# Performance work log

Measured on AMD Instinct MI355X. Metric: run time of the kernel, lower is better.

## Reference

```python
import jax, jax.numpy as jnp
import numpy as np

TOPK = 2
EPS = 1e-6  # RMSNorm epsilon


def setup_inputs() -> dict:
    key = jax.random.key(0)
    ks = jax.random.split(key, 8)
    b, t, d, h, n = 2, 1024, 1024, 2048, 16
    x = jax.random.normal(ks[0], (b, t, d), dtype=jnp.float32)
    router_w = jax.random.normal(ks[1], (n, d), dtype=jnp.float32) * (1.0 / np.sqrt(d))
    router_bias = jnp.zeros((n,), dtype=jnp.float32)
    bank_mag = jax.random.normal(ks[2], (n, d, h), dtype=jnp.float32) * (1.0 / np.sqrt(d))
    bank_freq = jax.random.uniform(ks[3], (n, d, h), dtype=jnp.float32, minval=0.5, maxval=2.0) * (1.0 / np.sqrt(d))
    bank_phase = jax.random.uniform(ks[4], (n, h), dtype=jnp.float32, minval=-0.3, maxval=0.3)
    bank_down = jax.random.normal(ks[5], (n, h, d), dtype=jnp.float32) * (1.0 / np.sqrt(h))
    norm_w = jnp.ones((d,), dtype=jnp.float32)
    return {
        'x': x, 'router_w': router_w, 'router_bias': router_bias,
        'bank_mag': bank_mag, 'bank_freq': bank_freq, 'bank_phase': bank_phase,
        'bank_down': bank_down, 'norm_w': norm_w,
    }


def reference(x, router_w, router_bias, bank_mag, bank_freq, bank_phase, bank_down, norm_w):
    b, t, d = x.shape
    # Router: scores [b,t,n], top-k selection, softmax over selected logits
    scores = jnp.einsum('btd,nd->btn', x, router_w) + router_bias
    topv, topi = jax.lax.top_k(scores, TOPK)            # [b,t,k]
    weights = jax.nn.softmax(topv, axis=-1)             # [b,t,k]

    fx = x.reshape(b * t, d)                            # [T,d]
    # Dense per-expert compute (mathematically identical to per-token gather+bmm):
    mag = jnp.einsum('td,ndh->tnh', fx, bank_mag)       # [T,n,h]
    freq = jnp.einsum('td,ndh->tnh', fx, bank_freq)     # [T,n,h]
    hidden = jnp.tanh(mag) * jnp.cos(jax.nn.softplus(freq) + 0.1 + bank_phase[None, :, :])
    out_all = jnp.einsum('tnh,nhd->tnd', hidden, bank_down)  # [T,n,d]

    # Gather the top-k expert outputs per token and combine with routing weights
    ti = topi.reshape(b * t, TOPK)                      # [T,k]
    sel = jnp.take_along_axis(out_all, ti[:, :, None], axis=1)  # [T,k,d]
    out = jnp.einsum('tkd,tk->td', sel, weights.reshape(b * t, TOPK)).reshape(b, t, d)

    # RMSNorm
    out = out * jax.lax.rsqrt(jnp.mean(out * out, axis=-1, keepdims=True) + EPS) * norm_w
    return out
```

## Files before the change

kernel.cpp:

```cpp
#include <hip/hip_runtime.h>
#include <hip/hip_bf16.h>
#include <cstdint>
#include <cstddef>

#define TT 2048
#define DD 1024
#define HH 2048
#define NE 16
#define WM128 48
#define BW35 35

typedef __bf16 bf16x8 __attribute__((ext_vector_type(8)));
typedef float f32x4 __attribute__((ext_vector_type(4)));

__device__ __forceinline__ unsigned short f2bf(float f) {
  union { float f; unsigned u; } v; v.f = f;
  unsigned r = (v.u + 0x7FFFu + ((v.u >> 16) & 1u)) >> 16;
  return (unsigned short)r;
}
__device__ __forceinline__ float bf2f(unsigned short s) {
  union { unsigned u; float f; } v; v.u = ((unsigned)s) << 16;
  return v.f;
}
__device__ __forceinline__ unsigned packbf(float lo, float hi) {
  return (unsigned)f2bf(lo) | ((unsigned)f2bf(hi) << 16);
}

__device__ __forceinline__ void gl_lds16(const void* g, void* l) {
  __builtin_amdgcn_global_load_lds(
      (const __attribute__((address_space(1))) unsigned int*)g,
      (__attribute__((address_space(3))) unsigned int*)l, 16, 0, 0);
}

union U4 { unsigned int u[4]; bf16x8 v; };

__global__ __launch_bounds__(256) void k_router(
    const float* __restrict__ x, const float* __restrict__ rw,
    const float* __restrict__ rb, int* __restrict__ cnt,
    int* __restrict__ list_tok, int* __restrict__ rec,
    float* __restrict__ wrec, unsigned short* __restrict__ xbf) {
  const int t = blockIdx.x;
  __shared__ float xs[DD];
  __shared__ float part[256];
  __shared__ float sc[NE];
  const float* xr = x + (size_t)t * DD;
  for (int i = threadIdx.x; i < DD; i += 256) xs[i] = xr[i];
  __syncthreads();
  {
    int i = threadIdx.x * 4;
    ushort4 o = { f2bf(xs[i]), f2bf(xs[i + 1]), f2bf(xs[i + 2]), f2bf(xs[i + 3]) };
    *reinterpret_cast<ushort4*>(xbf + (size_t)t * DD + i) = o;
  }
  const int e = threadIdx.x >> 4, j = threadIdx.x & 15;
  const float* w = rw + (size_t)e * DD;
  float s = 0.f;
  for (int i = j; i < DD; i += 16) s += xs[i] * w[i];
  part[threadIdx.x] = s;
  __syncthreads();
  if (threadIdx.x < NE) {
    float v = rb[threadIdx.x];
    #pragma unroll
    for (int q = 0; q < 16; ++q) v += part[threadIdx.x * 16 + q];
    sc[threadIdx.x] = v;
  }
  __syncthreads();
  if (threadIdx.x == 0) {
    int e1 = 0; float v1 = sc[0];
    #pragma unroll
    for (int q = 1; q < NE; ++q) { if (sc[q] > v1) { v1 = sc[q]; e1 = q; } }
    int e2 = -1; float v2 = -3.4e38f;
    #pragma unroll
    for (int q = 0; q < NE; ++q) {
      if (q != e1 && sc[q] > v2) { v2 = sc[q]; e2 = q; }
    }
    float ex = expf(v2 - v1);
    float w1 = 1.f / (1.f + ex);
    float w2 = ex / (1.f + ex);
    int p1 = atomicAdd(&cnt[e1], 1);
    int p2 = atomicAdd(&cnt[e2], 1);
    list_tok[e1 * TT + p1] = t;
    list_tok[e2 * TT + p2] = t;
    rec[t * 4 + 0] = e1; rec[t * 4 + 1] = p1;
    rec[t * 4 + 2] = e2; rec[t * 4 + 3] = p2;
    wrec[t * 2 + 0] = w1; wrec[t * 2 + 1] = w2;
  }
}

__global__ void k_sched(const int* __restrict__ cnt, int* __restrict__ work128,
                        int* __restrict__ woff) {
  if (threadIdx.x == 0) {
    int o = 0, n1 = 0;
    for (int e = 0; e < NE; ++e) {
      int ce = cnt[e];
      int a = (ce + 127) >> 7;
      for (int mb = 0; mb < a; ++mb) { work128[n1 * 2] = e; work128[n1 * 2 + 1] = mb; ++n1; }
      woff[e] = o; o += ce;
    }
    for (int q = n1; q < WM128; ++q) { work128[q * 2] = -1; work128[q * 2 + 1] = 0; }
  }
}

__global__ __launch_bounds__(256, 2) void k_up(
    const unsigned short* __restrict__ xbf,
    const float* __restrict__ bmag,
    const float* __restrict__ bfreq,
    const float* __restrict__ bphase,
    const int* __restrict__ cnt, const int* __restrict__ list_tok,
    const int* __restrict__ work, const int* __restrict__ woff,
    unsigned short* __restrict__ hid) {
  const int e = work[blockIdx.x * 2 + 0];
  if (e < 0) return;
  const int mt = work[blockIdx.x * 2 + 1];
  const int nt = blockIdx.y;
  const int ce = cnt[e];
  const int off = woff[e];
  __shared__ unsigned short As[2][128][64];
  __shared__ unsigned int BuM[2][64 * BW35];
  __shared__ unsigned int BuF[2][64 * BW35];
  __shared__ int toks[128];
  const int tid = threadIdx.x;
  if (tid < 128) {
    int r = mt * 128 + tid;
    toks[tid] = list_tok[e * TT + (r < ce ? r : ce - 1)];
  }
  __syncthreads();
  const int w = tid >> 6, l = tid & 63;
  const int lhi = l >> 3, llo = l & 7;
  size_t abase[4]; int aoff[4];
  #pragma unroll
  for (int j = 0; j < 4; ++j) {
    int seg = w * 4 + j;
    int r = seg * 8 + lhi;
    abase[j] = (size_t)toks[r] * DD + (size_t)((llo ^ (r & 7)) * 8);
    aoff[j] = seg * 512 + l * 8;
  }
  const int n0 = nt * 64;
  const float* srcM = bmag  + (size_t)e * DD * HH + n0 + 4 * (tid & 15);
  const float* srcF = bfreq + (size_t)e * DD * HH + n0 + 4 * (tid & 15);
  int q2s[2], bw[2][4];
  #pragma unroll
  for (int s = 0; s < 2; ++s) {
    int idx = s * 256 + tid;
    int q2 = idx >> 4;
    q2s[s] = q2;
    #pragma unroll
    for (int i = 0; i < 4; ++i) bw[s][i] = (4 * (tid & 15) + i) * BW35 + q2;
  }
  const int wm = (w >> 1) * 64, wn = (w & 1) * 32;
  const int lr = l & 15, kg = l >> 4;
  const f32x4 zero = {0.f, 0.f, 0.f, 0.f};
  f32x4 accM[4][2], accF[4][2];
  #pragma unroll
  for (int a = 0; a < 4; ++a)
    #pragma unroll
    for (int b = 0; b < 2; ++b) { accM[a][b] = zero; accF[a][b] = zero; }

  float4 rm0[2], rm1[2], rf0[2], rf1[2];
  auto loadB = [&](int kt) {
    #pragma unroll
    for (int s = 0; s < 2; ++s) {
      const float* pM = srcM + (size_t)(kt * 64 + 2 * q2s[s]) * HH;
      const float* pF = srcF + (size_t)(kt * 64 + 2 * q2s[s]) * HH;
      rm0[s] = *reinterpret_cast<const float4*>(pM);
      rm1[s] = *reinterpret_cast<const float4*>(pM + HH);
      rf0[s] = *reinterpret_cast<const float4*>(pF);
      rf1[s] = *reinterpret_cast<const float4*>(pF + HH);
    }
  };
  auto writeB = [&](int buf) {
    #pragma unroll
    for (int s = 0; s < 2; ++s) {
      const float* m0 = reinterpret_cast<const float*>(&rm0[s]);
      const float* m1 = reinterpret_cast<const float*>(&rm1[s]);
      const float* f0 = reinterpret_cast<const float*>(&rf0[s]);
      const float* f1 = reinterpret_cast<const float*>(&rf1[s]);
      #pragma unroll
      for (int i = 0; i < 4; ++i) {
        BuM[buf][bw[s][i]] = packbf(m0[i], m1[i]);
        BuF[buf][bw[s][i]] = packbf(f0[i], f1[i]);
      }
    }
  };

  loadB(0);
  #pragma unroll
  for (int j = 0; j < 4; ++j) gl_lds16(xbf + abase[j], &As[0][0][0] + aoff[j]);
  writeB(0);
  __syncthreads();
  int buf = 0;
  for (int kt = 0; kt < DD / 64; ++kt) {
    const bool more = (kt + 1) < DD / 64;
    if (more) {
      #pragma unroll
      for (int j = 0; j < 4; ++j)
        gl_lds16(xbf + abase[j] + (kt + 1) * 64, &As[buf ^ 1][0][0] + aoff[j]);
      loadB(kt + 1);
    }
    #pragma unroll
    for (int ks = 0; ks < 2; ++ks) {
      bf16x8 av[4];
      #pragma unroll
      for (int fm = 0; fm < 4; ++fm) {
        int row = wm + fm * 16 + lr;
        int c = (ks * 4 + kg) ^ (row & 7);
        av[fm] = *reinterpret_cast<const bf16x8*>(&As[buf][row][c * 8]);
      }
      U4 tm[2], tf[2];
      #pragma unroll
      for (int fn = 0; fn < 2; ++fn) {
        const int nb = (wn + fn * 16 + lr) * BW35 + ks * 16 + kg * 4;
        #pragma unroll
        for (int j2 = 0; j2 < 4; ++j2) {
          tm[fn].u[j2] = BuM[buf][nb + j2];
          tf[fn].u[j2] = BuF[buf][nb + j2];
        }
      }
      #pragma unroll
      for (int fm = 0; fm < 4; ++fm)
        #pragma unroll
        for (int fn = 0; fn < 2; ++fn) {
          accM[fm][fn] = __builtin_amdgcn_mfma_f32_16x16x32_bf16(av[fm], tm[fn].v, accM[fm][fn], 0, 0, 0);
          accF[fm][fn] = __builtin_amdgcn_mfma_f32_16x16x32_bf16(av[fm], tf[fn].v, accF[fm][fn], 0, 0, 0);
        }
    }
    if (more) writeB(buf ^ 1);
    __syncthreads();
    buf ^= 1;
  }
  #pragma unroll
  for (int fn = 0; fn < 2; ++fn) {
    const int ng = n0 + wn + fn * 16 + lr;
    const float ph = bphase[e * HH + ng] + 0.1f;
    #pragma unroll
    for (int fm = 0; fm < 4; ++fm) {
      #pragma unroll
      for (int jj = 0; jj < 4; ++jj) {
        int m = mt * 128 + wm + fm * 16 + kg * 4 + jj;
        if (m < ce) {
          float mv = accM[fm][fn][jj];
          float fv = accF[fm][fn][jj];
          float exn = __expf(-fabsf(fv));
          float sp = fmaxf(fv, 0.f) + __logf(1.f + exn);
          float t2 = __expf(2.f * mv);
          float th = 1.f - 2.f / (t2 + 1.f);
          float hv = th * __cosf(sp + ph);
          hid[(size_t)(off + m) * HH + ng] = f2bf(hv);
        }
      }
    }
  }
}

__global__ __launch_bounds__(256, 3) void k_down(
    const unsigned short* __restrict__ hid,
    const float* __restrict__ bdown,
    const int* __restrict__ cnt,
    const int* __restrict__ work, const int* __restrict__ woff,
    unsigned short* __restrict__ op) {
  const int e = work[blockIdx.x * 2 + 0];
  if (e < 0) return;
  const int mt = work[blockIdx.x * 2 + 1];
  const int nt = blockIdx.y;
  const int ce = cnt[e];
  const int off = woff[e];
  __shared__ unsigned short As[2][128][64];
  __shared__ unsigned int Bu[2][64 * BW35];
  const int tid = threadIdx.x;
  const int w = tid >> 6, l = tid & 63;
  const int lhi = l >> 3, llo = l & 7;
  size_t abase[4]; int aoff[4];
  #pragma unroll
  for (int j = 0; j < 4; ++j) {
    int seg = w * 4 + j;
    int r = seg * 8 + lhi;
    int gr = mt * 128 + r; if (gr >= ce) gr = ce - 1;
    abase[j] = (size_t)(off + gr) * HH + (size_t)((llo ^ (r & 7)) * 8);
    aoff[j] = seg * 512 + l * 8;
  }
  const int n0 = nt * 64;
  const float* srcD = bdown + (size_t)e * HH * DD + n0 + 4 * (tid & 15);
  int q2s[2], bw[2][4];
  #pragma unroll
  for (int s = 0; s < 2; ++s) {
    int idx = s * 256 + tid;
    int q2 = idx >> 4;
    q2s[s] = q2;
    #pragma unroll
    for (int i = 0; i < 4; ++i) bw[s][i] = (4 * (tid & 15) + i) * BW35 + q2;
  }
  const int wm = (w >> 1) * 64, wn = (w & 1) * 32;
  const int lr = l & 15, kg = l >> 4;
  const f32x4 zero = {0.f, 0.f, 0.f, 0.f};
  f32x4 acc[4][2];
  #pragma unroll
  for (int a = 0; a < 4; ++a)
    #pragma unroll
    for (int b = 0; b < 2; ++b) acc[a][b] = zero;

  float4 rd0[2], rd1[2];
  auto loadB = [&](int kt) {
    #pragma unroll
    for (int s = 0; s < 2; ++s) {
      const float* pD = srcD + (size_t)(kt * 64 + 2 * q2s[s]) * DD;
      rd0[s] = *reinterpret_cast<const float4*>(pD);
      rd1[s] = *reinterpret_cast<const float4*>(pD + DD);
    }
  };
  auto writeB = [&](int buf) {
    #pragma unroll
    for (int s = 0; s < 2; ++s) {
      const float* d0 = reinterpret_cast<const float*>(&rd0[s]);
      const float* d1 = reinterpret_cast<const float*>(&rd1[s]);
      #pragma unroll
      for (int i = 0; i < 4; ++i) Bu[buf][bw[s][i]] = packbf(d0[i], d1[i]);
    }
  };

  loadB(0);
  #pragma unroll
  for (int j = 0; j < 4; ++j) gl_lds16(hid + abase[j], &As[0][0][0] + aoff[j]);
  writeB(0);
  __syncthreads();
  int buf = 0;
  for (int kt = 0; kt < HH / 64; ++kt) {
    const bool more = (kt + 1) < HH / 64;
    if (more) {
      #pragma unroll
      for (int j = 0; j < 4; ++j)
        gl_lds16(hid + abase[j] + (kt + 1) * 64, &As[buf ^ 1][0][0] + aoff[j]);
      loadB(kt + 1);
    }
    #pragma unroll
    for (int ks = 0; ks < 2; ++ks) {
      bf16x8 av[4];
      #pragma unroll
      for (int fm = 0; fm < 4; ++fm) {
        int row = wm + fm * 16 + lr;
        int c = (ks * 4 + kg) ^ (row & 7);
        av[fm] = *reinterpret_cast<const bf16x8*>(&As[buf][row][c * 8]);
      }
      U4 t[2];
      #pragma unroll
      for (int fn = 0; fn < 2; ++fn) {
        const int nb = (wn + fn * 16 + lr) * BW35 + ks * 16 + kg * 4;
        #pragma unroll
        for (int j2 = 0; j2 < 4; ++j2) t[fn].u[j2] = Bu[buf][nb + j2];
      }
      #pragma unroll
      for (int fm = 0; fm < 4; ++fm)
        #pragma unroll
        for (int fn = 0; fn < 2; ++fn)
          acc[fm][fn] = __builtin_amdgcn_mfma_f32_16x16x32_bf16(av[fm], t[fn].v, acc[fm][fn], 0, 0, 0);
    }
    if (more) writeB(buf ^ 1);
    __syncthreads();
    buf ^= 1;
  }
  #pragma unroll
  for (int fn = 0; fn < 2; ++fn) {
    const int ng = n0 + wn + fn * 16 + lr;
    #pragma unroll
    for (int fm = 0; fm < 4; ++fm) {
      #pragma unroll
      for (int jj = 0; jj < 4; ++jj) {
        int m = mt * 128 + wm + fm * 16 + kg * 4 + jj;
        if (m < ce)
          op[(size_t)(off + m) * DD + ng] = f2bf(acc[fm][fn][jj]);
      }
    }
  }
}

__global__ __launch_bounds__(256) void k_norm(
    const unsigned short* __restrict__ op, const int* __restrict__ woff,
    const int* __restrict__ rec, const float* __restrict__ wrec,
    const float* __restrict__ nw, float* __restrict__ out) {
  const int t = blockIdx.x;
  const int tid = threadIdx.x;
  __shared__ float red[4];
  const int e1 = rec[t * 4 + 0], p1 = rec[t * 4 + 1];
  const int e2 = rec[t * 4 + 2], p2 = rec[t * 4 + 3];
  const float w1 = wrec[t * 2 + 0], w2 = wrec[t * 2 + 1];
  const unsigned short* pa = op + (size_t)(woff[e1] + p1) * DD;
  const unsigned short* pb = op + (size_t)(woff[e2] + p2) * DD;
  float v[4]; float ss = 0.f;
  #pragma unroll
  for (int q = 0; q < 4; ++q) {
    int i = q * 256 + tid;
    v[q] = w1 * bf2f(pa[i]) + w2 * bf2f(pb[i]);
    ss += v[q] * v[q];
  }
  #pragma unroll
  for (int o = 32; o > 0; o >>= 1) ss += __shfl_xor(ss, o);
  if ((tid & 63) == 0) red[tid >> 6] = ss;
  __syncthreads();
  const float tot = red[0] + red[1] + red[2] + red[3];
  const float scl = rsqrtf(tot * (1.f / DD) + 1e-6f);
  #pragma unroll
  for (int q = 0; q < 4; ++q) {
    int i = q * 256 + tid;
    out[(size_t)t * DD + i] = v[q] * scl * nw[i];
  }
}

extern "C" void kernel_launch(void* const* d_in, const int* in_sizes, int n_in,
                              void* d_out, int out_size, void* d_ws, size_t ws_size,
                              hipStream_t stream) {
  const float* x      = (const float*)d_in[0];
  const float* rw     = (const float*)d_in[1];
  const float* rb     = (const float*)d_in[2];
  const float* bmag   = (const float*)d_in[3];
  const float* bfreq  = (const float*)d_in[4];
  const float* bphase = (const float*)d_in[5];
  const float* bdown  = (const float*)d_in[6];
  const float* nw     = (const float*)d_in[7];
  float* out = (float*)d_out;
  char* ws = (char*)d_ws;
  const size_t MB = 1024 * 1024;
  int*   cnt    = (int*)(ws + 0);
  int*   work1  = (int*)(ws + 128);
  int*   woff   = (int*)(ws + 2048);
  int*   list   = (int*)(ws + 4096);
  int*   rec    = (int*)(ws + 139264);
  float* wrec   = (float*)(ws + 172032);
  unsigned short* xbf = (unsigned short*)(ws + 1 * MB);
  unsigned short* hid = (unsigned short*)(ws + 5 * MB);
  unsigned short* op  = (unsigned short*)(ws + 21 * MB);

  hipMemsetAsync(cnt, 0, 64, stream);
  k_router<<<TT, 256, 0, stream>>>(x, rw, rb, cnt, list, rec, wrec, xbf);
  k_sched<<<1, 64, 0, stream>>>(cnt, work1, woff);
  k_up<<<dim3(WM128, HH / 64), 256, 0, stream>>>(xbf, bmag, bfreq, bphase,
                                                 cnt, list, work1, woff, hid);
  k_down<<<dim3(WM128, DD / 64), 256, 0, stream>>>(hid, bdown, cnt, work1, woff, op);
  k_norm<<<TT, 256, 0, stream>>>(op, woff, rec, wrec, nw, out);
}
```

Baseline: 294.7 us.

## Prefetch weight tiles two stages ahead with ping-pong registers and vmcnt barriers

Both expert GEMM kernels (up-projection mag/freq and down-projection) now keep two register sets of fp32 weight tiles, so global loads run two k-steps ahead instead of one. The loop is unrolled by two, alternating LDS buffers. A custom barrier waits only until the oldest loads complete (partial vmcnt) instead of draining all outstanding memory operations, so later prefetches stay in flight across the barrier. This costs more VGPRs for the extra staging registers and relies on hand-counted vmcnt values that must match the issue order.

```diff
diff --git a/kernel.cpp b/kernel.cpp
--- a/kernel.cpp
+++ b/kernel.cpp
@@ -33,6 +33,15 @@
 }
 
 union U4 { unsigned int u[4]; bf16x8 v; };
+
+#define BARRIER_N(N)                                            \
+  do {                                                          \
+    asm volatile("s_waitcnt vmcnt(" #N ")" ::: "memory");       \
+    asm volatile("s_waitcnt lgkmcnt(0)" ::: "memory");          \
+    __builtin_amdgcn_sched_barrier(0);                          \
+    __builtin_amdgcn_s_barrier();                               \
+    __builtin_amdgcn_sched_barrier(0);                          \
+  } while (0)
 
 __global__ __launch_bounds__(256) void k_router(
     const float* __restrict__ x, const float* __restrict__ rw,
@@ -137,14 +146,14 @@
   const int n0 = nt * 64;
   const float* srcM = bmag  + (size_t)e * DD * HH + n0 + 4 * (tid & 15);
   const float* srcF = bfreq + (size_t)e * DD * HH + n0 + 4 * (tid & 15);
-  int q2s[2], bw[2][4];
+  int q2s[2], bwv[2][4];
   #pragma unroll
   for (int s = 0; s < 2; ++s) {
     int idx = s * 256 + tid;
     int q2 = idx >> 4;
     q2s[s] = q2;
     #pragma unroll
-    for (int i = 0; i < 4; ++i) bw[s][i] = (4 * (tid & 15) + i) * BW35 + q2;
+    for (int i = 0; i < 4; ++i) bwv[s][i] = (4 * (tid & 15) + i) * BW35 + q2;
   }
   const int wm = (w >> 1) * 64, wn = (w & 1) * 32;
   const int lr = l & 15, kg = l >> 4;
@@ -155,47 +164,65 @@
     #pragma unroll
     for (int b = 0; b < 2; ++b) { accM[a][b] = zero; accF[a][b] = zero; }
 
-  float4 rm0[2], rm1[2], rf0[2], rf1[2];
-  auto loadB = [&](int kt) {
+  float4 Am0[2], Am1[2], Af0[2], Af1[2];
+  float4 Bm0[2], Bm1[2], Bf0[2], Bf1[2];
+
+  auto glA = [&](int kt, int buf) {
+    #pragma unroll
+    for (int j = 0; j < 4; ++j)
+      gl_lds16(xbf + abase[j] + kt * 64, &As[buf][0][0] + aoff[j]);
+  };
+  auto loadBA = [&](int kt) {
     #pragma unroll
     for (int s = 0; s < 2; ++s) {
       const float* pM = srcM + (size_t)(kt * 64 + 2 * q2s[s]) * HH;
       const float* pF = srcF + (size_t)(kt * 64 + 2 * q2s[s]) * HH;
-      rm0[s] = *reinterpret_cast<const float4*>(pM);
-      rm1[s] = *reinterpret_cast<const float4*>(pM + HH);
-      rf0[s] = *reinterpret_cast<const float4*>(pF);
-      rf1[s] = *reinterpret_cast<const float4*>(pF + HH);
-    }
-  };
-  auto writeB = [&](int buf) {
-    #pragma unroll
-    for (int s = 0; s < 2; ++s) {
-      const float* m0 = reinterpret_cast<const float*>(&rm0[s]);
-      const float* m1 = reinterpret_cast<const float*>(&rm1[s]);
-      const float* f0 = reinterpret_cast<const float*>(&rf0[s]);
-      const float* f1 = reinterpret_cast<const float*>(&rf1[s]);
+      Am0[s] = *reinterpret_cast<const float4*>(pM);
+      Am1[s] = *reinterpret_cast<const float4*>(pM + HH);
+      Af0[s] = *reinterpret_cast<const float4*>(pF);
+      Af1[s] = *reinterpret_cast<const float4*>(pF + HH);
+    }
+  };
+  auto loadBB = [&](int kt) {
+    #pragma unroll
+    for (int s = 0; s < 2; ++s) {
+      const float* pM = srcM + (size_t)(kt * 64 + 2 * q2s[s]) * HH;
+      const float* pF = srcF + (size_t)(kt * 64 + 2 * q2s[s]) * HH;
+      Bm0[s] = *reinterpret_cast<const float4*>(pM);
+      Bm1[s] = *reinterpret_cast<const float4*>(pM + HH);
+      Bf0[s] = *reinterpret_cast<const float4*>(pF);
+      Bf1[s] = *reinterpret_cast<const float4*>(pF + HH);
+    }
+  };
+  auto writeBA = [&](int buf) {
+    #pragma unroll
+    for (int s = 0; s < 2; ++s) {
+      const float* m0 = reinterpret_cast<const float*>(&Am0[s]);
+      const float* m1 = reinterpret_cast<const float*>(&Am1[s]);
+      const float* f0 = reinterpret_cast<const float*>(&Af0[s]);
+      const float* f1 = reinterpret_cast<const float*>(&Af1[s]);
       #pragma unroll
       for (int i = 0; i < 4; ++i) {
-        BuM[buf][bw[s][i]] = packbf(m0[i], m1[i]);
-        BuF[buf][bw[s][i]] = packbf(f0[i], f1[i]);
-      }
-    }
-  };
-
-  loadB(0);
-  #pragma unroll
-  for (int j = 0; j < 4; ++j) gl_lds16(xbf + abase[j], &As[0][0][0] + aoff[j]);
-  writeB(0);
-  __syncthreads();
-  int buf = 0;
-  for (int kt = 0; kt < DD / 64; ++kt) {
-    const bool more = (kt + 1) < DD / 64;
-    if (more) {
-      #pragma unroll
-      for (int j = 0; j < 4; ++j)
-        gl_lds16(xbf + abase[j] + (kt + 1) * 64, &As[buf ^ 1][0][0] + aoff[j]);
-      loadB(kt + 1);
-    }
+        BuM[buf][bwv[s][i]] = packbf(m0[i], m1[i]);
+        BuF[buf][bwv[s][i]] = packbf(f0[i], f1[i]);
+      }
+    }
+  };
+  auto writeBB = [&](int buf) {
+    #pragma unroll
+    for (int s = 0; s < 2; ++s) {
+      const float* m0 = reinterpret_cast<const float*>(&Bm0[s]);
+      const float* m1 = reinterpret_cast<const float*>(&Bm1[s]);
+      const float* f0 = reinterpret_cast<const float*>(&Bf0[s]);
+      const float* f1 = reinterpret_cast<const float*>(&Bf1[s]);
+      #pragma unroll
+      for (int i = 0; i < 4; ++i) {
+        BuM[buf][bwv[s][i]] = packbf(m0[i], m1[i]);
+        BuF[buf][bwv[s][i]] = packbf(f0[i], f1[i]);
+      }
+    }
+  };
+  auto compute = [&](int buf) {
     #pragma unroll
     for (int ks = 0; ks < 2; ++ks) {
       bf16x8 av[4];
@@ -223,9 +250,32 @@
           accF[fm][fn] = __builtin_amdgcn_mfma_f32_16x16x32_bf16(av[fm], tf[fn].v, accF[fm][fn], 0, 0, 0);
         }
     }
-    if (more) writeB(buf ^ 1);
-    __syncthreads();
-    buf ^= 1;
+  };
+
+  glA(0, 0);
+  __builtin_amdgcn_sched_barrier(0);
+  loadBA(0);
+  loadBB(1);
+  writeBA(0);
+  BARRIER_N(8);
+  for (int kt = 0; kt < 16; kt += 2) {
+    glA(kt + 1, 1);
+    __builtin_amdgcn_sched_barrier(0);
+    loadBA(kt + 2 < 16 ? kt + 2 : 15);
+    compute(0);
+    writeBB(1);
+    BARRIER_N(8);
+    const bool more = kt + 2 < 16;
+    if (more) {
+      glA(kt + 2, 0);
+      __builtin_amdgcn_sched_barrier(0);
+      loadBB(kt + 3 < 16 ? kt + 3 : 15);
+    }
+    compute(1);
+    if (more) {
+      writeBA(0);
+      BARRIER_N(8);
+    }
   }
   #pragma unroll
   for (int fn = 0; fn < 2; ++fn) {
@@ -279,14 +329,14 @@
   }
   const int n0 = nt * 64;
   const float* srcD = bdown + (size_t)e * HH * DD + n0 + 4 * (tid & 15);
-  int q2s[2], bw[2][4];
+  int q2s[2], bwv[2][4];
   #pragma unroll
   for (int s = 0; s < 2; ++s) {
     int idx = s * 256 + tid;
     int q2 = idx >> 4;
     q2s[s] = q2;
     #pragma unroll
-    for (int i = 0; i < 4; ++i) bw[s][i] = (4 * (tid & 15) + i) * BW35 + q2;
+    for (int i = 0; i < 4; ++i) bwv[s][i] = (4 * (tid & 15) + i) * BW35 + q2;
   }
   const int wm = (w >> 1) * 64, wn = (w & 1) * 32;
   const int lr = l & 15, kg = l >> 4;
@@ -297,39 +347,49 @@
     #pragma unroll
     for (int b = 0; b < 2; ++b) acc[a][b] = zero;
 
-  float4 rd0[2], rd1[2];
-  auto loadB = [&](int kt) {
+  float4 Ad0[2], Ad1[2];
+  float4 Bd0[2], Bd1[2];
+
+  auto glA = [&](int kt, int buf) {
+    #pragma unroll
+    for (int j = 0; j < 4; ++j)
+      gl_lds16(hid + abase[j] + kt * 64, &As[buf][0][0] + aoff[j]);
+  };
+  auto loadBA = [&](int kt) {
     #pragma unroll
     for (int s = 0; s < 2; ++s) {
       const float* pD = srcD + (size_t)(kt * 64 + 2 * q2s[s]) * DD;
-      rd0[s] = *reinterpret_cast<const float4*>(pD);
-      rd1[s] = *reinterpret_cast<const float4*>(pD + DD);
-    }
-  };
-  auto writeB = [&](int buf) {
-    #pragma unroll
-    for (int s = 0; s < 2; ++s) {
-      const float* d0 = reinterpret_cast<const float*>(&rd0[s]);
-      const float* d1 = reinterpret_cast<const float*>(&rd1[s]);
-      #pragma unroll
-      for (int i = 0; i < 4; ++i) Bu[buf][bw[s][i]] = packbf(d0[i], d1[i]);
-    }
-  };
-
-  loadB(0);
-  #pragma unroll
-  for (int j = 0; j < 4; ++j) gl_lds16(hid + abase[j], &As[0][0][0] + aoff[j]);
-  writeB(0);
-  __syncthreads();
-  int buf = 0;
-  for (int kt = 0; kt < HH / 64; ++kt) {
-    const bool more = (kt + 1) < HH / 64;
-    if (more) {
-      #pragma unroll
-      for (int j = 0; j < 4; ++j)
-        gl_lds16(hid + abase[j] + (kt + 1) * 64, &As[buf ^ 1][0][0] + aoff[j]);
-      loadB(kt + 1);
-    }
+      Ad0[s] = *reinterpret_cast<const float4*>(pD);
+      Ad1[s] = *reinterpret_cast<const float4*>(pD + DD);
+    }
+  };
+  auto loadBB = [&](int kt) {
+    #pragma unroll
+    for (int s = 0; s < 2; ++s) {
+      const float* pD = srcD + (size_t)(kt * 64 + 2 * q2s[s]) * DD;
+      Bd0[s] = *reinterpret_cast<const float4*>(pD);
+      Bd1[s] = *reinterpret_cast<const float4*>(pD + DD);
+    }
+  };
+  auto writeBA = [&](int buf) {
+    #pragma unroll
+    for (int s = 0; s < 2; ++s) {
+      const float* d0 = reinterpret_cast<const float*>(&Ad0[s]);
+      const float* d1 = reinterpret_cast<const float*>(&Ad1[s]);
+      #pragma unroll
+      for (int i = 0; i < 4; ++i) Bu[buf][bwv[s][i]] = packbf(d0[i], d1[i]);
+    }
+  };
+  auto writeBB = [&](int buf) {
+    #pragma unroll
+    for (int s = 0; s < 2; ++s) {
+      const float* d0 = reinterpret_cast<const float*>(&Bd0[s]);
+      const float* d1 = reinterpret_cast<const float*>(&Bd1[s]);
+      #pragma unroll
+      for (int i = 0; i < 4; ++i) Bu[buf][bwv[s][i]] = packbf(d0[i], d1[i]);
+    }
+  };
+  auto compute = [&](int buf) {
     #pragma unroll
     for (int ks = 0; ks < 2; ++ks) {
       bf16x8 av[4];
@@ -352,9 +412,32 @@
         for (int fn = 0; fn < 2; ++fn)
           acc[fm][fn] = __builtin_amdgcn_mfma_f32_16x16x32_bf16(av[fm], t[fn].v, acc[fm][fn], 0, 0, 0);
     }
-    if (more) writeB(buf ^ 1);
-    __syncthreads();
-    buf ^= 1;
+  };
+
+  glA(0, 0);
+  __builtin_amdgcn_sched_barrier(0);
+  loadBA(0);
+  loadBB(1);
+  writeBA(0);
+  BARRIER_N(4);
+  for (int kt = 0; kt < 32; kt += 2) {
+    glA(kt + 1, 1);
+    __builtin_amdgcn_sched_barrier(0);
+    loadBA(kt + 2 < 32 ? kt + 2 : 31);
+    compute(0);
+    writeBB(1);
+    BARRIER_N(4);
+    const bool more = kt + 2 < 32;
+    if (more) {
+      glA(kt + 2, 0);
+      __builtin_amdgcn_sched_barrier(0);
+      loadBB(kt + 3 < 32 ? kt + 3 : 31);
+    }
+    compute(1);
+    if (more) {
+      writeBA(0);
+      BARRIER_N(4);
+    }
   }
   #pragma unroll
   for (int fn = 0; fn < 2; ++fn) {
```

After: 289.9 us. About the same (-1.6%).
